# Optimization experiments

Hardware: AMD Instinct MI355X
Metric: run time of the kernel (lower is better)

## Reference

```python
import jax, jax.numpy as jnp
import numpy as np

N, M, D = 1024, 1024, 256

def setup_inputs() -> dict:
    key = jax.random.key(0)
    ks = jax.random.split(key, 10)
    s = 1.0 / np.sqrt(D)
    return {
        "f_r": jax.random.normal(ks[0], (N, D), jnp.float32),
        "f_r_prime": jax.random.normal(ks[1], (M, D), jnp.float32),
        "W_w": jax.random.uniform(ks[2], (D, D), jnp.float32, -s, s),
        "W_b": jax.random.uniform(ks[3], (D,), jnp.float32, -s, s),
        "Wp_w": jax.random.uniform(ks[4], (D, D), jnp.float32, -s, s),
        "Wp_b": jax.random.uniform(ks[5], (D,), jnp.float32, -s, s),
        "w_w": jax.random.uniform(ks[6], (1, D), jnp.float32, -s, s),
        "w_b": jax.random.uniform(ks[7], (1,), jnp.float32, -s, s),
        "wp_w": jax.random.uniform(ks[8], (1, D), jnp.float32, -s, s),
        "wp_b": jax.random.uniform(ks[9], (1,), jnp.float32, -s, s),
    }

def reference(f_r, f_r_prime, W_w, W_b, Wp_w, Wp_b, w_w, w_b, wp_w, wp_b):
    q = f_r @ W_w.T + W_b            # [N, D]
    k = f_r_prime @ Wp_w.T + Wp_b    # [M, D]
    # additive (Bahdanau) scores: tanh over broadcast sum [N, M, D]
    h = jnp.tanh(q[:, None, :] + k[None, :, :])
    alpha = h @ w_w.T + w_b          # [N, M, 1]
    alpha = jax.nn.softmax(alpha, axis=1)
    # stage-1 pooling over M (weights on raw f_r_prime, as in source)
    context = jnp.sum(alpha * f_r_prime[None, :, :], axis=1)  # [N, D]
    # stage-2 attention pooling over N
    alpha_p = jax.nn.softmax(context @ wp_w.T + wp_b, axis=0)  # [N, 1]
    pool = jnp.sum(alpha_p * context, axis=0, keepdims=True)   # [1, D]
    return pool
```

## Files before the change

kernel.cpp:

```cpp
#include <hip/hip_runtime.h>

#define NN 1024
#define MM 1024
#define DD 256

typedef float floatx2 __attribute__((ext_vector_type(2)));

__device__ __forceinline__ float rcp_fast(float x) { return __builtin_amdgcn_rcpf(x); }

__global__ __launch_bounds__(256) void gemm_exp_kernel(
    const float* __restrict__ f_r,  const float* __restrict__ W_w,  const float* __restrict__ W_b,
    const float* __restrict__ f_rp, const float* __restrict__ Wp_w, const float* __restrict__ Wp_b,
    float* __restrict__ Eq, float* __restrict__ EkT, float* __restrict__ out0)
{
    __shared__ float As[32][36];
    __shared__ float Bs[32][68];
    __shared__ float T[64][36];

    const int b = blockIdx.x;
    const int t = threadIdx.x;
    if (b == 0) out0[t] = 0.f;

    const int mat  = b >> 7;
    const int tile = b & 127;
    const int rt = tile & 31, dt = tile >> 5;
    const float* __restrict__ A    = mat ? f_rp : f_r;
    const float* __restrict__ B    = mat ? Wp_w : W_w;
    const float* __restrict__ bias = mat ? Wp_b : W_b;

    const int tx = t & 15, ty = t >> 4;
    const int r0 = rt * 32, d0 = dt * 64;
    const int ar = t >> 3, ak = (t & 7) * 4;
    const int br = t >> 2, bk = (t & 3) * 8;

    float acc[2][4];
    #pragma unroll
    for (int i = 0; i < 2; ++i)
        #pragma unroll
        for (int j = 0; j < 4; ++j) acc[i][j] = 0.f;

    for (int kk = 0; kk < DD; kk += 32) {
        float4 av  = *(const float4*)(A + (size_t)(r0 + ar) * DD + kk + ak);
        float4 bv0 = *(const float4*)(B + (size_t)(d0 + br) * DD + kk + bk);
        float4 bv1 = *(const float4*)(B + (size_t)(d0 + br) * DD + kk + bk + 4);
        __syncthreads();
        As[ak + 0][ar] = av.x; As[ak + 1][ar] = av.y; As[ak + 2][ar] = av.z; As[ak + 3][ar] = av.w;
        Bs[bk + 0][br] = bv0.x; Bs[bk + 1][br] = bv0.y; Bs[bk + 2][br] = bv0.z; Bs[bk + 3][br] = bv0.w;
        Bs[bk + 4][br] = bv1.x; Bs[bk + 5][br] = bv1.y; Bs[bk + 6][br] = bv1.z; Bs[bk + 7][br] = bv1.w;
        __syncthreads();
        #pragma unroll
        for (int k = 0; k < 32; ++k) {
            float2 a2 = *(const float2*)&As[k][ty * 2];
            float4 b4 = *(const float4*)&Bs[k][tx * 4];
            float aa[2] = {a2.x, a2.y};
            float bb[4] = {b4.x, b4.y, b4.z, b4.w};
            #pragma unroll
            for (int i = 0; i < 2; ++i)
                #pragma unroll
                for (int j = 0; j < 4; ++j)
                    acc[i][j] = fmaf(aa[i], bb[j], acc[i][j]);
        }
    }

    float bj[4];
    #pragma unroll
    for (int j = 0; j < 4; ++j) bj[j] = bias[d0 + tx * 4 + j];

    float e[2][4];
    #pragma unroll
    for (int i = 0; i < 2; ++i)
        #pragma unroll
        for (int j = 0; j < 4; ++j) {
            float v = acc[i][j] + bj[j];
            v = fminf(fmaxf(v, -5.f), 5.f);
            e[i][j] = __expf(2.f * v);
        }

    if (mat == 0) {
        #pragma unroll
        for (int i = 0; i < 2; ++i)
            *(float4*)&Eq[(size_t)(r0 + ty * 2 + i) * DD + d0 + tx * 4] =
                make_float4(e[i][0], e[i][1], e[i][2], e[i][3]);
    } else {
        __syncthreads();
        #pragma unroll
        for (int i = 0; i < 2; ++i)
            #pragma unroll
            for (int j = 0; j < 4; ++j) T[tx * 4 + j][ty * 2 + i] = e[i][j];
        __syncthreads();
        const int dl = t >> 3, rl = (t & 7) * 4;
        #pragma unroll
        for (int h = 0; h < 2; ++h) {
            int dloc = dl + 32 * h;
            float4 tv = *(const float4*)&T[dloc][rl];
            *(float4*)&EkT[(size_t)(d0 + dloc) * MM + r0 + rl] = tv;
        }
    }
}

__global__ __launch_bounds__(1024, 4) void fused_attn_kernel(
    const float* __restrict__ Eq, const float* __restrict__ EkT,
    const float* __restrict__ w_w, const float* __restrict__ frp,
    const float* __restrict__ wp_w,
    float* __restrict__ ctxA, float* __restrict__ ctxB,
    float* __restrict__ SpA, float* __restrict__ SpB,
    float* __restrict__ sA,  float* __restrict__ sB)
{
    __shared__ __align__(16) char usm_raw[65536];
    float2 (*accbuf2)[4][256] = (float2 (*)[4][256])(void*)usm_raw;
    float4 (*ctxred)[4][64]   = (float4 (*)[4][64])(void*)usm_raw;
    __shared__ float alsm[4][512];
    __shared__ float redsm[4][4];
    __shared__ float redsc[16];

    const int t  = threadIdx.x;
    const int tg = t >> 7;
    const int tm = t & 127;
    const int bm = blockIdx.x & 1;
    const int n0 = (blockIdx.x >> 1) * 4;
    const int m0 = bm * 512;

    const int dh = __builtin_amdgcn_readfirstlane(tg * 32);
    const float* __restrict__ eqb = Eq + (size_t)n0 * DD + dh;
    const float* __restrict__ wwb = w_w + dh;

    const floatx2 one2 = {1.f, 1.f};
    floatx2 accl[4] = {{0.f,0.f},{0.f,0.f},{0.f,0.f},{0.f,0.f}};
    floatx2 acch[4] = {{0.f,0.f},{0.f,0.f},{0.f,0.f},{0.f,0.f}};

    const float* ekb = EkT + (size_t)dh * MM + m0 + 4 * tm;

    for (int gi = 0; gi < 8; ++gi) {
        const float* nb = ekb + (size_t)(gi * 4) * MM;
        float4 c0 = *(const float4*)(nb + 0 * MM);
        float4 c1 = *(const float4*)(nb + 1 * MM);
        float4 c2 = *(const float4*)(nb + 2 * MM);
        float4 c3 = *(const float4*)(nb + 3 * MM);
        const int db = gi * 4;
        float4 w4 = *(const float4*)(wwb + db);
        floatx2 kv[4][2] = {{{c0.x, c0.y}, {c0.z, c0.w}},
                            {{c1.x, c1.y}, {c1.z, c1.w}},
                            {{c2.x, c2.y}, {c2.z, c2.w}},
                            {{c3.x, c3.y}, {c3.z, c3.w}}};
        #pragma unroll
        for (int n = 0; n < 4; ++n) {
            float4 q4 = *(const float4*)(eqb + n * DD + db);
            #pragma unroll
            for (int h = 0; h < 2; ++h) {
                floatx2 x0 = q4.x * kv[0][h] + one2;
                floatx2 x1 = q4.y * kv[1][h] + one2;
                floatx2 x2 = q4.z * kv[2][h] + one2;
                floatx2 x3 = q4.w * kv[3][h] + one2;
                floatx2 p01 = x0 * x1;
                floatx2 p23 = x2 * x3;
                floatx2 n01 = w4.x * x1 + w4.y * x0;
                floatx2 n23 = w4.z * x3 + w4.w * x2;
                floatx2 nc  = n01 * p23 + n23 * p01;
                floatx2 pt  = p01 * p23;
                floatx2 r;  r.x = rcp_fast(pt.x);  r.y = rcp_fast(pt.y);
                if (h == 0) accl[n] += nc * r; else acch[n] += nc * r;
            }
        }
    }

    #pragma unroll
    for (int n = 0; n < 4; ++n)
        *(float4*)&accbuf2[tg][n][2 * tm] =
            make_float4(accl[n].x, accl[n].y, acch[n].x, acch[n].y);
    __syncthreads();

    const int bn = t >> 8, j = t & 255;
    const int w4id = (t >> 6) & 3;
    const int lane = t & 63;
    float2 aj = make_float2(0.f, 0.f);
    #pragma unroll
    for (int g8 = 0; g8 < 8; ++g8) {
        float2 v = accbuf2[g8][bn][j];
        aj.x += v.x; aj.y += v.y;
    }
    float ex = __expf(-2.f * aj.x), ey = __expf(-2.f * aj.y);
    *(float2*)&alsm[bn][2 * j] = make_float2(ex, ey);
    float sm = ex + ey;
    #pragma unroll
    for (int off = 32; off > 0; off >>= 1) sm += __shfl_xor(sm, off);
    if (lane == 0) redsm[bn][w4id] = sm;
    __syncthreads();
    if (j == 0) {
        float* Sp = bm ? SpB : SpA;
        Sp[n0 + bn] = redsm[bn][0] + redsm[bn][1] + redsm[bn][2] + redsm[bn][3];
    }

    const int cc = t & 63;
    const int rr = t >> 6;
    floatx2 axl[4] = {{0.f,0.f},{0.f,0.f},{0.f,0.f},{0.f,0.f}};
    floatx2 axh[4] = {{0.f,0.f},{0.f,0.f},{0.f,0.f},{0.f,0.f}};
    const float* fb = frp + (size_t)(m0 + rr * 32) * DD + 4 * cc;
    for (int m8 = 0; m8 < 8; ++m8) {
        float alv[4][4];
        #pragma unroll
        for (int n = 0; n < 4; ++n) {
            float4 a4 = *(const float4*)&alsm[n][rr * 32 + m8 * 4];
            alv[n][0] = a4.x; alv[n][1] = a4.y; alv[n][2] = a4.z; alv[n][3] = a4.w;
        }
        #pragma unroll
        for (int mm = 0; mm < 4; ++mm) {
            float4 f = *(const float4*)(fb + (size_t)(m8 * 4 + mm) * DD);
            floatx2 fl = {f.x, f.y}, fh = {f.z, f.w};
            #pragma unroll
            for (int n = 0; n < 4; ++n) {
                axl[n] += alv[n][mm] * fl;
                axh[n] += alv[n][mm] * fh;
            }
        }
    }
    #pragma unroll
    for (int n = 0; n < 4; ++n)
        ctxred[rr][n][cc] = make_float4(axl[n].x, axl[n].y, axh[n].x, axh[n].y);
    __syncthreads();

    const int nn = t >> 8, d = t & 255;
    float s = 0.f;
    #pragma unroll
    for (int r = 0; r < 16; ++r)
        s += ((const float*)&ctxred[r][nn][d >> 2])[d & 3];
    float* ctxP = bm ? ctxB : ctxA;
    ctxP[(size_t)(n0 + nn) * DD + d] = s;

    float p = s * wp_w[d];
    #pragma unroll
    for (int off = 32; off > 0; off >>= 1) p += __shfl_xor(p, off);
    if (lane == 0) redsc[t >> 6] = p;
    __syncthreads();
    if (t < 4) {
        float* sP = bm ? sB : sA;
        sP[n0 + t] = redsc[4 * t] + redsc[4 * t + 1] + redsc[4 * t + 2] + redsc[4 * t + 3];
    }
}

__global__ __launch_bounds__(256) void pool_kernel(
    const float* __restrict__ ctxA, const float* __restrict__ ctxB,
    const float* __restrict__ SpA,  const float* __restrict__ SpB,
    const float* __restrict__ sA,   const float* __restrict__ sB,
    float* __restrict__ out)
{
    __shared__ float red[8];
    const int t = threadIdx.x, lane = t & 63, wid = t >> 6;
    const int n0 = blockIdx.x * 4;

    float sc[4];
    #pragma unroll
    for (int i = 0; i < 4; ++i) {
        int r = t + 256 * i;
        sc[i] = (sA[r] + sB[r]) * rcp_fast(SpA[r] + SpB[r]);
    }
    float mx = fmaxf(fmaxf(sc[0], sc[1]), fmaxf(sc[2], sc[3]));
    #pragma unroll
    for (int off = 32; off > 0; off >>= 1) mx = fmaxf(mx, __shfl_xor(mx, off));
    if (lane == 0) red[wid] = mx;
    __syncthreads();
    mx = fmaxf(fmaxf(red[0], red[1]), fmaxf(red[2], red[3]));

    float se = __expf(sc[0] - mx) + __expf(sc[1] - mx) + __expf(sc[2] - mx) + __expf(sc[3] - mx);
    #pragma unroll
    for (int off = 32; off > 0; off >>= 1) se += __shfl_xor(se, off);
    if (lane == 0) red[4 + wid] = se;
    __syncthreads();
    se = red[4] + red[5] + red[6] + red[7];
    float invS = rcp_fast(se);

    float racc = 0.f;
    #pragma unroll
    for (int i = 0; i < 4; ++i) {
        int row = n0 + i;
        float invRow = rcp_fast(SpA[row] + SpB[row]);
        float scr = (sA[row] + sB[row]) * invRow;
        float ap = __expf(scr - mx) * invS;
        float cr = (ctxA[(size_t)row * DD + t] + ctxB[(size_t)row * DD + t]) * invRow;
        racc = fmaf(ap, cr, racc);
    }
    atomicAdd(out + t, racc);
}

extern "C" void kernel_launch(void* const* d_in, const int* in_sizes, int n_in,
                              void* d_out, int out_size, void* d_ws, size_t ws_size,
                              hipStream_t stream) {
    const float* f_r  = (const float*)d_in[0];
    const float* f_rp = (const float*)d_in[1];
    const float* W_w  = (const float*)d_in[2];
    const float* W_b  = (const float*)d_in[3];
    const float* Wp_w = (const float*)d_in[4];
    const float* Wp_b = (const float*)d_in[5];
    const float* w_w  = (const float*)d_in[6];
    const float* wp_w = (const float*)d_in[8];
    float* out = (float*)d_out;

    float* ws    = (float*)d_ws;
    float* Eq    = ws;
    float* EkT   = ws + 262144;
    float* ctxA  = ws + 524288;
    float* ctxB  = ws + 786432;
    float* SpA   = ws + 1048576;
    float* SpB   = ws + 1049600;
    float* sA    = ws + 1050624;
    float* sB    = ws + 1051648;

    gemm_exp_kernel<<<256, 256, 0, stream>>>(f_r, W_w, W_b, f_rp, Wp_w, Wp_b, Eq, EkT, out);
    fused_attn_kernel<<<512, 1024, 0, stream>>>(Eq, EkT, w_w, f_rp, wp_w,
                                                ctxA, ctxB, SpA, SpB, sA, sB);
    pool_kernel<<<256, 256, 0, stream>>>(ctxA, ctxB, SpA, SpB, sA, sB, out);
}
```

Before: 124.2 us.

## Interleave Ek by d-quads, pack along d with scalar-operand pk_fma

Stores the exponentiated key projection as d-quad-interleaved blocks (each m holds 4 consecutive d values) instead of a plain transpose. The attention kernel then assigns one m per thread with two d-halves per block, and uses inline-asm v_pk_fma/v_pk_mul with wave-uniform q and w operands held in SGPRs. Products are merged over 8 d values per reciprocal instead of 4. This halves the rcp count and the cross-group shared-memory reduction. The risk is a larger dynamic range in the 8-term product denominators, and inline asm that may constrain the scheduler.

```diff
diff --git a/kernel.cpp b/kernel.cpp
--- a/kernel.cpp
+++ b/kernel.cpp
@@ -8,14 +8,35 @@
 
 __device__ __forceinline__ float rcp_fast(float x) { return __builtin_amdgcn_rcpf(x); }
 
+__device__ __forceinline__ floatx2 pk_mul(floatx2 a, floatx2 b) {
+    floatx2 d;
+    asm("v_pk_mul_f32 %0, %1, %2" : "=v"(d) : "v"(a), "v"(b));
+    return d;
+}
+__device__ __forceinline__ floatx2 pk_fma(floatx2 a, floatx2 b, floatx2 c) {
+    floatx2 d;
+    asm("v_pk_fma_f32 %0, %1, %2, %3" : "=v"(d) : "v"(a), "v"(b), "v"(c));
+    return d;
+}
+__device__ __forceinline__ floatx2 pk_mul_vs(floatx2 a, floatx2 b) {
+    floatx2 d;
+    asm("v_pk_mul_f32 %0, %1, %2" : "=v"(d) : "v"(a), "s"(b));
+    return d;
+}
+__device__ __forceinline__ floatx2 pk_fma_vs(floatx2 a, floatx2 b, floatx2 c) {
+    floatx2 d;
+    asm("v_pk_fma_f32 %0, %1, %2, %3" : "=v"(d) : "v"(a), "s"(b), "v"(c));
+    return d;
+}
+
 __global__ __launch_bounds__(256) void gemm_exp_kernel(
     const float* __restrict__ f_r,  const float* __restrict__ W_w,  const float* __restrict__ W_b,
     const float* __restrict__ f_rp, const float* __restrict__ Wp_w, const float* __restrict__ Wp_b,
-    float* __restrict__ Eq, float* __restrict__ EkT, float* __restrict__ out0)
+    float* __restrict__ Eq, float* __restrict__ Ek4, float* __restrict__ out0)
 {
     __shared__ float As[32][36];
     __shared__ float Bs[32][68];
-    __shared__ float T[64][36];
+    __shared__ float4 T4[32][17];
 
     const int b = blockIdx.x;
     const int t = threadIdx.x;
@@ -85,21 +106,20 @@
         __syncthreads();
         #pragma unroll
         for (int i = 0; i < 2; ++i)
-            #pragma unroll
-            for (int j = 0; j < 4; ++j) T[tx * 4 + j][ty * 2 + i] = e[i][j];
+            T4[ty * 2 + i][tx] = make_float4(e[i][0], e[i][1], e[i][2], e[i][3]);
         __syncthreads();
-        const int dl = t >> 3, rl = (t & 7) * 4;
+        const int sm = t & 31, sq = t >> 5;
         #pragma unroll
         for (int h = 0; h < 2; ++h) {
-            int dloc = dl + 32 * h;
-            float4 tv = *(const float4*)&T[dloc][rl];
-            *(float4*)&EkT[(size_t)(d0 + dloc) * MM + r0 + rl] = tv;
+            const int dql = sq + 8 * h;
+            float4 v = T4[sm][dql];
+            *(float4*)&Ek4[(size_t)((d0 >> 2) + dql) * (4 * MM) + (size_t)(r0 + sm) * 4] = v;
         }
     }
 }
 
 __global__ __launch_bounds__(1024, 4) void fused_attn_kernel(
-    const float* __restrict__ Eq, const float* __restrict__ EkT,
+    const float* __restrict__ Eq, const float* __restrict__ Ek4,
     const float* __restrict__ w_w, const float* __restrict__ frp,
     const float* __restrict__ wp_w,
     float* __restrict__ ctxA, float* __restrict__ ctxB,
@@ -107,78 +127,71 @@
     float* __restrict__ sA,  float* __restrict__ sB)
 {
     __shared__ __align__(16) char usm_raw[65536];
-    float2 (*accbuf2)[4][256] = (float2 (*)[4][256])(void*)usm_raw;
-    float4 (*ctxred)[4][64]   = (float4 (*)[4][64])(void*)usm_raw;
+    float (*part)[4][512]   = (float (*)[4][512])(void*)usm_raw;
+    float4 (*ctxred)[4][64] = (float4 (*)[4][64])(void*)usm_raw;
     __shared__ float alsm[4][512];
     __shared__ float redsm[4][4];
     __shared__ float redsc[16];
 
-    const int t  = threadIdx.x;
-    const int tg = t >> 7;
-    const int tm = t & 127;
-    const int bm = blockIdx.x & 1;
-    const int n0 = (blockIdx.x >> 1) * 4;
-    const int m0 = bm * 512;
-
-    const int dh = __builtin_amdgcn_readfirstlane(tg * 32);
-    const float* __restrict__ eqb = Eq + (size_t)n0 * DD + dh;
-    const float* __restrict__ wwb = w_w + dh;
+    const int t   = threadIdx.x;
+    const int m_l = t & 511;
+    const int tg  = t >> 9;
+    const int bm  = blockIdx.x & 1;
+    const int n0  = (blockIdx.x >> 1) * 4;
+    const int m0  = bm * 512;
+
+    const int dbase = __builtin_amdgcn_readfirstlane(tg * 128);
+    const float* __restrict__ eqb = Eq + (size_t)n0 * DD + dbase;
+    const float* __restrict__ wwb = w_w + dbase;
+    const float* __restrict__ ekb = Ek4 + (size_t)(dbase >> 2) * (4 * MM) + (size_t)(m0 + m_l) * 4;
 
     const floatx2 one2 = {1.f, 1.f};
-    floatx2 accl[4] = {{0.f,0.f},{0.f,0.f},{0.f,0.f},{0.f,0.f}};
-    floatx2 acch[4] = {{0.f,0.f},{0.f,0.f},{0.f,0.f},{0.f,0.f}};
-
-    const float* ekb = EkT + (size_t)dh * MM + m0 + 4 * tm;
-
-    for (int gi = 0; gi < 8; ++gi) {
-        const float* nb = ekb + (size_t)(gi * 4) * MM;
-        float4 c0 = *(const float4*)(nb + 0 * MM);
-        float4 c1 = *(const float4*)(nb + 1 * MM);
-        float4 c2 = *(const float4*)(nb + 2 * MM);
-        float4 c3 = *(const float4*)(nb + 3 * MM);
-        const int db = gi * 4;
-        float4 w4 = *(const float4*)(wwb + db);
-        floatx2 kv[4][2] = {{{c0.x, c0.y}, {c0.z, c0.w}},
-                            {{c1.x, c1.y}, {c1.z, c1.w}},
-                            {{c2.x, c2.y}, {c2.z, c2.w}},
-                            {{c3.x, c3.y}, {c3.z, c3.w}}};
+    floatx2 acc[4] = {{0.f,0.f},{0.f,0.f},{0.f,0.f},{0.f,0.f}};
+
+    for (int c8 = 0; c8 < 16; ++c8) {
+        float4 ekA = *(const float4*)(ekb + (size_t)(2 * c8 + 0) * (4 * MM));
+        float4 ekB = *(const float4*)(ekb + (size_t)(2 * c8 + 1) * (4 * MM));
+        floatx2 ek01 = {ekA.x, ekA.y}, ek23 = {ekA.z, ekA.w};
+        floatx2 ek45 = {ekB.x, ekB.y}, ek67 = {ekB.z, ekB.w};
+        const int db = c8 * 8;
+        floatx2 w01 = *(const floatx2*)(wwb + db + 0);
+        floatx2 w23 = *(const floatx2*)(wwb + db + 2);
+        floatx2 w45 = *(const floatx2*)(wwb + db + 4);
+        floatx2 w67 = *(const floatx2*)(wwb + db + 6);
         #pragma unroll
         for (int n = 0; n < 4; ++n) {
-            float4 q4 = *(const float4*)(eqb + n * DD + db);
-            #pragma unroll
-            for (int h = 0; h < 2; ++h) {
-                floatx2 x0 = q4.x * kv[0][h] + one2;
-                floatx2 x1 = q4.y * kv[1][h] + one2;
-                floatx2 x2 = q4.z * kv[2][h] + one2;
-                floatx2 x3 = q4.w * kv[3][h] + one2;
-                floatx2 p01 = x0 * x1;
-                floatx2 p23 = x2 * x3;
-                floatx2 n01 = w4.x * x1 + w4.y * x0;
-                floatx2 n23 = w4.z * x3 + w4.w * x2;
-                floatx2 nc  = n01 * p23 + n23 * p01;
-                floatx2 pt  = p01 * p23;
-                floatx2 r;  r.x = rcp_fast(pt.x);  r.y = rcp_fast(pt.y);
-                if (h == 0) accl[n] += nc * r; else acch[n] += nc * r;
-            }
+            const float* qn = eqb + (size_t)n * DD + db;
+            floatx2 q01 = *(const floatx2*)(qn + 0);
+            floatx2 q23 = *(const floatx2*)(qn + 2);
+            floatx2 q45 = *(const floatx2*)(qn + 4);
+            floatx2 q67 = *(const floatx2*)(qn + 6);
+            floatx2 x01 = pk_fma_vs(ek01, q01, one2);
+            floatx2 x23 = pk_fma_vs(ek23, q23, one2);
+            floatx2 x45 = pk_fma_vs(ek45, q45, one2);
+            floatx2 x67 = pk_fma_vs(ek67, q67, one2);
+            floatx2 den1 = pk_mul(x01, x23);
+            floatx2 num1 = pk_fma_vs(x01, w23, pk_mul_vs(x23, w01));
+            floatx2 den2 = pk_mul(x45, x67);
+            floatx2 num2 = pk_fma_vs(x45, w67, pk_mul_vs(x67, w45));
+            floatx2 DEN = pk_mul(den1, den2);
+            floatx2 NUM = pk_fma(num2, den1, pk_mul(num1, den2));
+            floatx2 r2; r2.x = rcp_fast(DEN.x); r2.y = rcp_fast(DEN.y);
+            acc[n] = pk_fma(NUM, r2, acc[n]);
         }
     }
 
     #pragma unroll
     for (int n = 0; n < 4; ++n)
-        *(float4*)&accbuf2[tg][n][2 * tm] =
-            make_float4(accl[n].x, accl[n].y, acch[n].x, acch[n].y);
+        part[tg][n][m_l] = acc[n].x + acc[n].y;
     __syncthreads();
 
     const int bn = t >> 8, j = t & 255;
     const int w4id = (t >> 6) & 3;
     const int lane = t & 63;
-    float2 aj = make_float2(0.f, 0.f);
-    #pragma unroll
-    for (int g8 = 0; g8 < 8; ++g8) {
-        float2 v = accbuf2[g8][bn][j];
-        aj.x += v.x; aj.y += v.y;
-    }
-    float ex = __expf(-2.f * aj.x), ey = __expf(-2.f * aj.y);
+    float2 a0 = *(const float2*)&part[0][bn][2 * j];
+    float2 a1 = *(const float2*)&part[1][bn][2 * j];
+    float sx = a0.x + a1.x, sy = a0.y + a1.y;
+    float ex = __expf(-2.f * sx), ey = __expf(-2.f * sy);
     *(float2*)&alsm[bn][2 * j] = make_float2(ex, ey);
     float sm = ex + ey;
     #pragma unroll
@@ -296,7 +309,7 @@
 
     float* ws    = (float*)d_ws;
     float* Eq    = ws;
-    float* EkT   = ws + 262144;
+    float* Ek4   = ws + 262144;
     float* ctxA  = ws + 524288;
     float* ctxB  = ws + 786432;
     float* SpA   = ws + 1048576;
@@ -304,8 +317,8 @@
     float* sA    = ws + 1050624;
     float* sB    = ws + 1051648;
 
-    gemm_exp_kernel<<<256, 256, 0, stream>>>(f_r, W_w, W_b, f_rp, Wp_w, Wp_b, Eq, EkT, out);
-    fused_attn_kernel<<<512, 1024, 0, stream>>>(Eq, EkT, w_w, f_rp, wp_w,
+    gemm_exp_kernel<<<256, 256, 0, stream>>>(f_r, W_w, W_b, f_rp, Wp_w, Wp_b, Eq, Ek4, out);
+    fused_attn_kernel<<<512, 1024, 0, stream>>>(Eq, Ek4, w_w, f_rp, wp_w,
                                                 ctxA, ctxB, SpA, SpB, sA, sB);
     pool_kernel<<<256, 256, 0, stream>>>(ctxA, ctxB, SpA, SpB, sA, sB, out);
 }
```

Result: no change. 121.8 us (-1.9%).
